# Kernel tuning notes

Measured on AMD Instinct MI355X. Metric: run time of the kernel, lower is better.

Reference implementation:

```python
import jax, jax.numpy as jnp
import numpy as np

R = 16            # grid resolution
WIN = 8           # window size (voxels per side)
NW3 = (R // WIN) ** 3   # number of windows = 8
WS = WIN ** 3           # tokens per window = 512
N = R ** 3              # active voxels = 4096
C = 512; H = 8; DH = C // H; L = 8; LAT = 8
NG = 4; VOX = 0.015625; OUTC = 14 * NG; MLP = 4 * C


def _radical_inverse(base, i):
    f = 1.0; r = 0.0
    while i > 0:
        f /= base; r += f * (i % base); i //= base
    return r


def _offset_perturbation():
    # hammersley_sequence(3, i, NG) = [i/NG, phi_2(i), phi_3(i)]
    p = np.array([[i / NG, _radical_inverse(2, i), _radical_inverse(3, i)] for i in range(NG)], np.float32)
    p = p * 2.0 - 1.0
    p = np.clip(p / VOX, -0.99, 0.99)
    return jnp.asarray(np.arctanh(p).astype(np.float32))  # [NG, 3]


def setup_inputs() -> dict:
    key = jax.random.key(0)
    ks = jax.random.split(key, 12)
    nw = R // WIN
    # window-major voxel ordering: dense 16^3 grid grouped into 8^3 windows
    win = np.stack(np.meshgrid(*[np.arange(nw)] * 3, indexing='ij'), -1).reshape(-1, 3)
    inner = np.stack(np.meshgrid(*[np.arange(WIN)] * 3, indexing='ij'), -1).reshape(-1, 3)
    xyz = (win[:, None, :] * WIN + inner[None, :, :]).reshape(-1, 3).astype(np.int32)
    coords = jnp.asarray(np.concatenate([np.zeros((N, 1), np.int32), xyz], axis=1))  # [N,4] (batch,x,y,z)
    s = 0.02
    return {
        'feats': jax.random.normal(ks[0], (N, LAT), jnp.float32),
        'coords': coords,
        'emb_x': jax.random.normal(ks[1], (1024, C // 3), jnp.float32) * s,
        'emb_y': jax.random.normal(ks[2], (1024, C // 3), jnp.float32) * s,
        'emb_z': jax.random.normal(ks[3], (1024, C - 2 * (C // 3)), jnp.float32) * s,
        'w_in': jax.random.normal(ks[4], (LAT, C), jnp.float32) * s,
        'b_in': jnp.zeros((C,), jnp.float32),
        'ln1_g': jnp.ones((L, C), jnp.float32), 'ln1_b': jnp.zeros((L, C), jnp.float32),
        'w_qkv': jax.random.normal(ks[5], (L, C, 3 * C), jnp.float32) * s,
        'b_qkv': jnp.zeros((L, 3 * C), jnp.float32),
        'w_o': jax.random.normal(ks[6], (L, C, C), jnp.float32) * s,
        'b_o': jnp.zeros((L, C), jnp.float32),
        'ln2_g': jnp.ones((L, C), jnp.float32), 'ln2_b': jnp.zeros((L, C), jnp.float32),
        'w_m1': jax.random.normal(ks[7], (L, C, MLP), jnp.float32) * s,
        'b_m1': jnp.zeros((L, MLP), jnp.float32),
        'w_m2': jax.random.normal(ks[8], (L, MLP, C), jnp.float32) * s,
        'b_m2': jnp.zeros((L, C), jnp.float32),
        'w_out': jax.random.normal(ks[9], (C, OUTC), jnp.float32) * s,
        'b_out': jnp.zeros((OUTC,), jnp.float32),
        'offset_perturb': _offset_perturbation(),
    }


def _ln(x, g, b, eps):
    m = jnp.mean(x, axis=-1, keepdims=True)
    v = jnp.var(x, axis=-1, keepdims=True)
    return (x - m) * jax.lax.rsqrt(v + eps) * g + b


def _forward(feats, coords, emb_x, emb_y, emb_z, w_in, b_in, ln1_g, ln1_b,
             w_qkv, b_qkv, w_o, b_o, ln2_g, ln2_b, w_m1, b_m1, w_m2, b_m2,
             w_out, b_out, offset_perturb):
    # input_layer + absolute position embedding (gather from 3 tables)
    h = feats @ w_in + b_in  # [N, C]
    pe = jnp.concatenate([emb_x[coords[:, 1]], emb_y[coords[:, 2]], emb_z[coords[:, 3]]], axis=-1)
    h = h + pe

    def block(h, p):
        l1g, l1b, wq, bq, wo, bo, l2g, l2b, w1, b1, w2, b2 = p
        a = _ln(h, l1g, l1b, 1e-6)
        qkv = (a @ wq + bq).reshape(NW3, WS, 3, H, DH)  # voxels are window-major
        q, k, v = qkv[:, :, 0], qkv[:, :, 1], qkv[:, :, 2]
        scores = jnp.einsum('wqhd,wkhd->whqk', q, k) / jnp.sqrt(jnp.float32(DH))
        attn = jax.nn.softmax(scores, axis=-1)
        o = jnp.einsum('whqk,wkhd->wqhd', attn, v).reshape(N, C)
        h = h + o @ wo + bo
        m = _ln(h, l2g, l2b, 1e-6)
        h = h + jax.nn.gelu(m @ w1 + b1) @ w2 + b2
        return h, None

    params = (ln1_g, ln1_b, w_qkv, b_qkv, w_o, b_o, ln2_g, ln2_b, w_m1, b_m1, w_m2, b_m2)
    h, _ = jax.lax.scan(block, h, params)

    # final non-affine layer_norm + out projection
    h = _ln(h, jnp.ones((C,), h.dtype), jnp.zeros((C,), h.dtype), 1e-5)
    out = h @ w_out + b_out  # [N, 56]

    # to_representation (single batch)
    xyz_base = (coords[:, 1:].astype(jnp.float32) + 0.5) / R  # [N, 3]
    off = out[:, 0:3 * NG].reshape(N, NG, 3) + offset_perturb
    off = jnp.tanh(off) / R * 0.5 * VOX
    _xyz = (xyz_base[:, None, :] + off).reshape(N * NG, 3)
    _fdc = out[:, 3 * NG:6 * NG].reshape(N * NG, 1, 3)
    _scal = out[:, 6 * NG:9 * NG].reshape(N * NG, 3)
    _rot = out[:, 9 * NG:13 * NG].reshape(N * NG, 4)
    _opa = out[:, 13 * NG:14 * NG].reshape(N * NG, 1)
    return _xyz, _fdc, _scal, _rot, _opa


def reference(feats, coords, emb_x, emb_y, emb_z, w_in, b_in, ln1_g, ln1_b,
              w_qkv, b_qkv, w_o, b_o, ln2_g, ln2_b, w_m1, b_m1, w_m2, b_m2,
              w_out, b_out, offset_perturb):
    return _forward(feats, coords, emb_x, emb_y, emb_z, w_in, b_in, ln1_g, ln1_b,
                    w_qkv, b_qkv, w_o, b_o, ln2_g, ln2_b, w_m1, b_m1, w_m2, b_m2,
                    w_out, b_out, offset_perturb)
```

## Files before the change

### kernel.cpp

```cpp
#include <hip/hip_runtime.h>
#include <stdint.h>

typedef unsigned short u16;
typedef short bf16x8 __attribute__((ext_vector_type(8)));
typedef float f32x4 __attribute__((ext_vector_type(4)));

#define NTOK 4096
#define CDIM 512
#define NHEAD 8
#define LAYERS 8
#define MLPD 2048
#define QKVD 1536

__device__ __forceinline__ u16 f2bf(float f){
  union { float f; unsigned u; } c; c.f = f;
  return (u16)((c.u + 0x7FFFu + ((c.u >> 16) & 1u)) >> 16);
}

__device__ __forceinline__ unsigned pack2(float a, float b){
  return (unsigned)f2bf(a) | ((unsigned)f2bf(b) << 16);
}

__device__ __forceinline__ void llds16(const void* g, void* l){
  __builtin_amdgcn_global_load_lds((const __attribute__((address_space(1))) void*)g,
                                   (__attribute__((address_space(3))) void*)l, 16, 0, 0);
}

__global__ void kt_transpose(const float* __restrict__ W, u16* __restrict__ Wt, int K, int N){
  __shared__ float tile[32][33];
  int l = blockIdx.z;
  W  += (size_t)l * K * N;
  Wt += (size_t)l * K * N;
  int k0 = blockIdx.y * 32, n0 = blockIdx.x * 32;
  int t = threadIdx.x;
  int r = t >> 3, c4 = (t & 7) << 2;
  float4 v = *(const float4*)&W[(size_t)(k0 + r) * N + n0 + c4];
  tile[r][c4 + 0] = v.x; tile[r][c4 + 1] = v.y; tile[r][c4 + 2] = v.z; tile[r][c4 + 3] = v.w;
  __syncthreads();
  ushort4 o;
  o.x = f2bf(tile[c4 + 0][r]);
  o.y = f2bf(tile[c4 + 1][r]);
  o.z = f2bf(tile[c4 + 2][r]);
  o.w = f2bf(tile[c4 + 3][r]);
  *(ushort4*)&Wt[(size_t)(n0 + r) * K + k0 + c4] = o;
}

__global__ void kt_embed(const float* __restrict__ feats, const int* __restrict__ coords,
                         const float* __restrict__ ex, const float* __restrict__ ey,
                         const float* __restrict__ ez, const float* __restrict__ w_in,
                         const float* __restrict__ b_in, float* __restrict__ h){
  __shared__ float fs[8];
  __shared__ int cc[3];
  int n = blockIdx.x, t = threadIdx.x;
  if (t < 8) fs[t] = feats[n * 8 + t];
  if (t == 8) { cc[0] = coords[n*4+1]; cc[1] = coords[n*4+2]; cc[2] = coords[n*4+3]; }
  __syncthreads();
  for (int c = t; c < CDIM; c += 256){
    float acc = b_in[c];
    #pragma unroll
    for (int i = 0; i < 8; i++) acc += fs[i] * w_in[i * CDIM + c];
    float pe;
    if (c < 170)      pe = ex[cc[0] * 170 + c];
    else if (c < 340) pe = ey[cc[1] * 170 + (c - 170)];
    else              pe = ez[cc[2] * 172 + (c - 340)];
    h[(size_t)n * CDIM + c] = acc + pe;
  }
}

__global__ void kt_ln(const float* __restrict__ h, const float* __restrict__ g,
                      const float* __restrict__ b, u16* __restrict__ out, float eps){
  int wave = threadIdx.x >> 6, lane = threadIdx.x & 63;
  int row = blockIdx.x * 4 + wave;
  const float* hr = h + (size_t)row * CDIM + lane * 8;
  float4 v0 = *(const float4*)hr, v1 = *(const float4*)(hr + 4);
  float x[8] = {v0.x, v0.y, v0.z, v0.w, v1.x, v1.y, v1.z, v1.w};
  float s = 0.f, q = 0.f;
  #pragma unroll
  for (int i = 0; i < 8; i++){ s += x[i]; q += x[i] * x[i]; }
  #pragma unroll
  for (int off = 32; off; off >>= 1){ s += __shfl_xor(s, off); q += __shfl_xor(q, off); }
  float mean = s * (1.0f / CDIM);
  float var  = q * (1.0f / CDIM) - mean * mean;
  float rr = rsqrtf(var + eps);
  int cb = lane * 8;
  u16 u[8];
  #pragma unroll
  for (int i = 0; i < 8; i++)
    u[i] = f2bf((x[i] - mean) * rr * g[cb + i] + b[cb + i]);
  uint4 pk;
  pk.x = (unsigned)u[0] | ((unsigned)u[1] << 16);
  pk.y = (unsigned)u[2] | ((unsigned)u[3] << 16);
  pk.z = (unsigned)u[4] | ((unsigned)u[5] << 16);
  pk.w = (unsigned)u[6] | ((unsigned)u[7] << 16);
  *(uint4*)&out[(size_t)row * CDIM + cb] = pk;
}

template<int BM, int BN, int MODE>
__global__ __launch_bounds__(256) void kt_gemm(
    const u16* __restrict__ A, const u16* __restrict__ Wt, const float* __restrict__ bias,
    u16* __restrict__ outb, float* __restrict__ hres, u16* __restrict__ vT, int N, int K)
{
  constexpr int MF = BM / 32;
  constexpr int NF = BN / 32;
  __shared__ __align__(16) u16 As[2][BM * 64];
  __shared__ __align__(16) u16 Bs[2][BN * 64];
  int tid = threadIdx.x, wave = tid >> 6, lane = tid & 63;
  int m0 = blockIdx.y * BM, n0 = blockIdx.x * BN;
  int wm = wave >> 1, wn = wave & 1;
  f32x4 acc[MF][NF];
  const f32x4 fzero = {0.f, 0.f, 0.f, 0.f};
  #pragma unroll
  for (int m = 0; m < MF; m++)
    #pragma unroll
    for (int n = 0; n < NF; n++) acc[m][n] = fzero;

  int srow = lane >> 3;
  int sblk = (lane & 7) ^ srow;
  const u16* gA = A  + (size_t)(m0 + wave * 8 + srow) * K + sblk * 8;
  const u16* gB = Wt + (size_t)(n0 + wave * 8 + srow) * K + sblk * 8;

  auto stage = [&](int buf, int kt){
    #pragma unroll
    for (int j = 0; j < BM / 32; j++)
      llds16(gA + (size_t)(j * 32) * K + kt, &As[buf][(j * 32 + wave * 8) * 64]);
    #pragma unroll
    for (int j = 0; j < BN / 32; j++)
      llds16(gB + (size_t)(j * 32) * K + kt, &Bs[buf][(j * 32 + wave * 8) * 64]);
  };

  int nk = K >> 6;
  stage(0, 0);
  __syncthreads();
  int rl = lane & 15, hg = lane >> 4;
  for (int t = 0; t < nk; ++t){
    int cur = t & 1;
    if (t + 1 < nk) stage(cur ^ 1, (t + 1) << 6);
    #pragma unroll
    for (int kk = 0; kk < 2; kk++){
      bf16x8 af[MF], bfr[NF];
      int bl = (kk << 2) + hg;
      #pragma unroll
      for (int m = 0; m < MF; m++){
        int row = wm * (BM / 2) + m * 16 + rl;
        af[m] = *(const bf16x8*)&As[cur][row * 64 + ((bl ^ (row & 7)) << 3)];
      }
      #pragma unroll
      for (int n = 0; n < NF; n++){
        int row = wn * (BN / 2) + n * 16 + rl;
        bfr[n] = *(const bf16x8*)&Bs[cur][row * 64 + ((bl ^ (row & 7)) << 3)];
      }
      #pragma unroll
      for (int m = 0; m < MF; m++)
        #pragma unroll
        for (int n = 0; n < NF; n++)
          acc[m][n] = __builtin_amdgcn_mfma_f32_16x16x32_bf16(af[m], bfr[n], acc[m][n], 0, 0, 0);
    }
    __syncthreads();
  }

  int cl = lane & 15, rg = lane >> 4;
  #pragma unroll
  for (int m = 0; m < MF; m++){
    int row0 = m0 + wm * (BM / 2) + m * 16 + rg * 4;
    #pragma unroll
    for (int n = 0; n < NF; n++){
      int col = n0 + wn * (BN / 2) + n * 16 + cl;
      float bb = bias[col];
      if (MODE == 1){
        #pragma unroll
        for (int r = 0; r < 4; r++){
          size_t idx = (size_t)(row0 + r) * N + col;
          hres[idx] += acc[m][n][r] + bb;
        }
      } else if (MODE == 2){
        #pragma unroll
        for (int r = 0; r < 4; r++){
          float x = acc[m][n][r] + bb;
          float t = 0.7978845608028654f * (x + 0.044715f * x * x * x);
          outb[(size_t)(row0 + r) * N + col] = f2bf(0.5f * x * (1.0f + tanhf(t)));
        }
      } else {
        if (col < 1024){
          #pragma unroll
          for (int r = 0; r < 4; r++)
            outb[(size_t)(row0 + r) * N + col] = f2bf(acc[m][n][r] + bb);
        } else {
          int dh = col - 1024;
          int win = row0 >> 9, tin = row0 & 511;
          ushort4 p;
          p.x = f2bf(acc[m][n][0] + bb);
          p.y = f2bf(acc[m][n][1] + bb);
          p.z = f2bf(acc[m][n][2] + bb);
          p.w = f2bf(acc[m][n][3] + bb);
          *(ushort4*)&vT[(size_t)(win * 512 + dh) * 512 + tin] = p;
        }
      }
    }
  }
}

__global__ __launch_bounds__(256) void kt_attn(const u16* __restrict__ qkv,
                                               const u16* __restrict__ vT,
                                               u16* __restrict__ o){
  int tid = threadIdx.x, wave = tid >> 6, lane = tid & 63;
  int task = blockIdx.x * 4 + wave;
  int qc = task & 31, head = (task >> 5) & 7, win = task >> 8;
  int rl = lane & 15, hg = lane >> 4;
  int qbase = win * 512 + qc * 16;
  const u16* qptr = qkv + (size_t)(qbase + rl) * QKVD + head * 64;
  const u16* kptr = qkv + (size_t)(win * 512) * QKVD + 512 + head * 64;
  const u16* vptr = vT + (size_t)(win * 512 + head * 64) * 512;

  bf16x8 qf0 = *(const bf16x8*)(qptr + hg * 8);
  bf16x8 qf1 = *(const bf16x8*)(qptr + 32 + hg * 8);

  const f32x4 fzero = {0.f, 0.f, 0.f, 0.f};
  f32x4 Oa[4] = {fzero, fzero, fzero, fzero};
  float mrun = -1e30f, lrun = 0.f;

  bf16x8 kA[2][2], vA[4], kB[2][2], vB[4];

  auto loadK = [&](int kt, bf16x8 kf[2][2]){
    #pragma unroll
    for (int c = 0; c < 2; c++)
      #pragma unroll
      for (int dk = 0; dk < 2; dk++)
        kf[c][dk] = *(const bf16x8*)(kptr + (size_t)(kt + c * 16 + rl) * QKVD + dk * 32 + hg * 8);
  };
  auto loadV = [&](int kt, bf16x8 vf[4]){
    #pragma unroll
    for (int d = 0; d < 4; d++)
      vf[d] = *(const bf16x8*)(vptr + (size_t)(d * 16 + rl) * 512 + kt + hg * 8);
  };

  auto process = [&](bf16x8 kf[2][2], bf16x8 vf[4]){
    f32x4 s0 = fzero, s1 = fzero;
    s0 = __builtin_amdgcn_mfma_f32_16x16x32_bf16(kf[0][0], qf0, s0, 0, 0, 0);
    s0 = __builtin_amdgcn_mfma_f32_16x16x32_bf16(kf[0][1], qf1, s0, 0, 0, 0);
    s1 = __builtin_amdgcn_mfma_f32_16x16x32_bf16(kf[1][0], qf0, s1, 0, 0, 0);
    s1 = __builtin_amdgcn_mfma_f32_16x16x32_bf16(kf[1][1], qf1, s1, 0, 0, 0);
    float v[8];
    #pragma unroll
    for (int r = 0; r < 4; r++){ v[r] = s0[r] * 0.125f; v[4 + r] = s1[r] * 0.125f; }
    float tmax = v[0];
    #pragma unroll
    for (int i = 1; i < 8; i++) tmax = fmaxf(tmax, v[i]);
    tmax = fmaxf(tmax, __shfl_xor(tmax, 16));
    tmax = fmaxf(tmax, __shfl_xor(tmax, 32));
    float mnew = fmaxf(mrun, tmax);
    float corr = __expf(mrun - mnew);
    mrun = mnew;
    float p[8], ps = 0.f;
    #pragma unroll
    for (int i = 0; i < 8; i++){ p[i] = __expf(v[i] - mnew); ps += p[i]; }
    ps += __shfl_xor(ps, 16);
    ps += __shfl_xor(ps, 32);
    lrun = lrun * corr + ps;
    float c0 = __shfl(corr, (hg << 2) + 0);
    float c1 = __shfl(corr, (hg << 2) + 1);
    float c2 = __shfl(corr, (hg << 2) + 2);
    float c3 = __shfl(corr, (hg << 2) + 3);
    #pragma unroll
    for (int d = 0; d < 4; d++){
      Oa[d][0] *= c0; Oa[d][1] *= c1; Oa[d][2] *= c2; Oa[d][3] *= c3;
    }
    unsigned pk00 = pack2(p[0], p[1]);
    unsigned pk01 = pack2(p[2], p[3]);
    unsigned pk10 = pack2(p[4], p[5]);
    unsigned pk11 = pack2(p[6], p[7]);
    int idx0 = rl | ((( hg << 1)      & 3) << 4);
    int idx1 = rl | ((((hg << 1) + 1) & 3) << 4);
    bool hiC = hg >= 2;
    unsigned W0a = __shfl(pk00, idx0), W0b = __shfl(pk10, idx0);
    unsigned W1a = __shfl(pk01, idx0), W1b = __shfl(pk11, idx0);
    unsigned W2a = __shfl(pk00, idx1), W2b = __shfl(pk10, idx1);
    unsigned W3a = __shfl(pk01, idx1), W3b = __shfl(pk11, idx1);
    uint4 W;
    W.x = hiC ? W0b : W0a;
    W.y = hiC ? W1b : W1a;
    W.z = hiC ? W2b : W2a;
    W.w = hiC ? W3b : W3a;
    bf16x8 pf;
    __builtin_memcpy(&pf, &W, 16);
    #pragma unroll
    for (int d = 0; d < 4; d++)
      Oa[d] = __builtin_amdgcn_mfma_f32_16x16x32_bf16(pf, vf[d], Oa[d], 0, 0, 0);
  };

  loadK(0, kA); loadV(0, vA);
  for (int kt = 0; kt < 512; kt += 64){
    loadK(kt + 32, kB); loadV(kt + 32, vB);
    process(kA, vA);
    if (kt + 64 < 512){ loadK(kt + 64, kA); loadV(kt + 64, vA); }
    process(kB, vB);
  }

  float l0 = __shfl(lrun, (hg << 2) + 0);
  float l1 = __shfl(lrun, (hg << 2) + 1);
  float l2 = __shfl(lrun, (hg << 2) + 2);
  float l3 = __shfl(lrun, (hg << 2) + 3);
  float li[4] = {1.f / l0, 1.f / l1, 1.f / l2, 1.f / l3};
  #pragma unroll
  for (int d = 0; d < 4; d++)
    #pragma unroll
    for (int r = 0; r < 4; r++){
      int row = qbase + (hg << 2) + r;
      o[(size_t)row * CDIM + head * 64 + d * 16 + rl] = f2bf(Oa[d][r] * li[r]);
    }
}

__global__ void kt_final(const float* __restrict__ h, const float* __restrict__ w_out,
                         const float* __restrict__ b_out, const int* __restrict__ coords,
                         const float* __restrict__ offp, float* __restrict__ out){
  __shared__ float lnv[CDIM];
  __shared__ float ov[56];
  int n = blockIdx.x, lane = threadIdx.x;
  const float* hr = h + (size_t)n * CDIM + lane * 8;
  float4 v0 = *(const float4*)hr, v1 = *(const float4*)(hr + 4);
  float x[8] = {v0.x, v0.y, v0.z, v0.w, v1.x, v1.y, v1.z, v1.w};
  float s = 0.f, q = 0.f;
  #pragma unroll
  for (int i = 0; i < 8; i++){ s += x[i]; q += x[i] * x[i]; }
  #pragma unroll
  for (int off = 32; off; off >>= 1){ s += __shfl_xor(s, off); q += __shfl_xor(q, off); }
  float mean = s * (1.0f / CDIM);
  float var  = q * (1.0f / CDIM) - mean * mean;
  float rr = rsqrtf(var + 1e-5f);
  #pragma unroll
  for (int i = 0; i < 8; i++) lnv[lane * 8 + i] = (x[i] - mean) * rr;
  __syncthreads();
  if (lane < 56){
    float a = b_out[lane];
    for (int k = 0; k < CDIM; k++) a += lnv[k] * w_out[k * 56 + lane];
    ov[lane] = a;
  }
  __syncthreads();
  if (lane < 12){
    int g = lane / 3, d = lane - g * 3;
    float base = ((float)coords[n * 4 + 1 + d] + 0.5f) * (1.0f / 16.0f);
    float t = tanhf(ov[lane] + offp[lane]);
    out[(size_t)n * 12 + lane] = base + t * 4.8828125e-4f;
    out[49152  + (size_t)n * 12 + lane] = ov[12 + lane];
    out[98304  + (size_t)n * 12 + lane] = ov[24 + lane];
  }
  if (lane < 16) out[147456 + (size_t)n * 16 + lane] = ov[36 + lane];
  if (lane < 4)  out[212992 + (size_t)n * 4  + lane] = ov[52 + lane];
}

extern "C" void kernel_launch(void* const* d_in, const int* in_sizes, int n_in,
                              void* d_out, int out_size, void* d_ws, size_t ws_size,
                              hipStream_t stream) {
  const float* feats = (const float*)d_in[0];
  const int*   coords = (const int*)d_in[1];
  const float* emb_x = (const float*)d_in[2];
  const float* emb_y = (const float*)d_in[3];
  const float* emb_z = (const float*)d_in[4];
  const float* w_in  = (const float*)d_in[5];
  const float* b_in  = (const float*)d_in[6];
  const float* ln1_g = (const float*)d_in[7];
  const float* ln1_b = (const float*)d_in[8];
  const float* w_qkv = (const float*)d_in[9];
  const float* b_qkv = (const float*)d_in[10];
  const float* w_o   = (const float*)d_in[11];
  const float* b_o   = (const float*)d_in[12];
  const float* ln2_g = (const float*)d_in[13];
  const float* ln2_b = (const float*)d_in[14];
  const float* w_m1  = (const float*)d_in[15];
  const float* b_m1  = (const float*)d_in[16];
  const float* w_m2  = (const float*)d_in[17];
  const float* b_m2  = (const float*)d_in[18];
  const float* w_out = (const float*)d_in[19];
  const float* b_out = (const float*)d_in[20];
  const float* offp  = (const float*)d_in[21];

  char* ws = (char*)d_ws;
  auto carve = [&](size_t bytes){ char* p = ws; ws += (bytes + 255) & ~(size_t)255; return p; };
  float* h   = (float*)carve((size_t)NTOK * CDIM * 4);
  u16* a     = (u16*)carve((size_t)NTOK * CDIM * 2);
  u16* qkvb  = (u16*)carve((size_t)NTOK * QKVD * 2);
  u16* vT    = (u16*)carve((size_t)NTOK * CDIM * 2);
  u16* ob    = (u16*)carve((size_t)NTOK * CDIM * 2);
  u16* ub    = (u16*)carve((size_t)NTOK * MLPD * 2);
  u16* wqkvT = (u16*)carve((size_t)LAYERS * QKVD * CDIM * 2);
  u16* woT   = (u16*)carve((size_t)LAYERS * CDIM * CDIM * 2);
  u16* wm1T  = (u16*)carve((size_t)LAYERS * MLPD * CDIM * 2);
  u16* wm2T  = (u16*)carve((size_t)LAYERS * CDIM * MLPD * 2);

  kt_transpose<<<dim3(QKVD/32, CDIM/32, LAYERS), 256, 0, stream>>>(w_qkv, wqkvT, CDIM, QKVD);
  kt_transpose<<<dim3(CDIM/32, CDIM/32, LAYERS), 256, 0, stream>>>(w_o,   woT,   CDIM, CDIM);
  kt_transpose<<<dim3(MLPD/32, CDIM/32, LAYERS), 256, 0, stream>>>(w_m1,  wm1T,  CDIM, MLPD);
  kt_transpose<<<dim3(CDIM/32, MLPD/32, LAYERS), 256, 0, stream>>>(w_m2,  wm2T,  MLPD, CDIM);
  kt_embed<<<NTOK, 256, 0, stream>>>(feats, coords, emb_x, emb_y, emb_z, w_in, b_in, h);

  for (int l = 0; l < LAYERS; ++l){
    kt_ln<<<NTOK/4, 256, 0, stream>>>(h, ln1_g + l*CDIM, ln1_b + l*CDIM, a, 1e-6f);
    kt_gemm<64,128,0><<<dim3(QKVD/128, NTOK/64), 256, 0, stream>>>(
        a, wqkvT + (size_t)l*QKVD*CDIM, b_qkv + l*QKVD, qkvb, nullptr, vT, QKVD, CDIM);
    kt_attn<<<512, 256, 0, stream>>>(qkvb, vT, ob);
    kt_gemm<64,64,1><<<dim3(CDIM/64, NTOK/64), 256, 0, stream>>>(
        ob, woT + (size_t)l*CDIM*CDIM, b_o + l*CDIM, nullptr, h, nullptr, CDIM, CDIM);
    kt_ln<<<NTOK/4, 256, 0, stream>>>(h, ln2_g + l*CDIM, ln2_b + l*CDIM, a, 1e-6f);
    kt_gemm<64,128,2><<<dim3(MLPD/128, NTOK/64), 256, 0, stream>>>(
        a, wm1T + (size_t)l*MLPD*CDIM, b_m1 + l*MLPD, ub, nullptr, nullptr, MLPD, CDIM);
    kt_gemm<64,64,1><<<dim3(CDIM/64, NTOK/64), 256, 0, stream>>>(
        ub, wm2T + (size_t)l*CDIM*MLPD, b_m2 + l*CDIM, nullptr, h, nullptr, CDIM, MLPD);
  }
  kt_final<<<NTOK, 64, 0, stream>>>(h, w_out, b_out, coords, offp, (float*)d_out);
}
```

Measured before the change: 978.3 us.

## Triple-buffer GEMM LDS pipeline and stage attention K/V through shared memory

The GEMM moves from double to triple buffering in LDS. It waits with explicit vmcnt counters and a single barrier per k-step instead of two __syncthreads. The attention kernel now groups four waves of one head and window per block. Those waves share K/V tiles loaded into swizzled LDS through a triple-buffered async global_load_lds pipeline, replacing per-wave redundant global register loads. This is meant to cut redundant global traffic and barrier stalls, at the cost of more LDS use and reliance on hand-tuned vmcnt correctness.

```diff
diff --git a/kernel.cpp b/kernel.cpp
--- a/kernel.cpp
+++ b/kernel.cpp
@@ -24,6 +24,14 @@
 __device__ __forceinline__ void llds16(const void* g, void* l){
   __builtin_amdgcn_global_load_lds((const __attribute__((address_space(1))) void*)g,
                                    (__attribute__((address_space(3))) void*)l, 16, 0, 0);
+}
+
+template<int N> __device__ __forceinline__ void wait_vmcnt(){
+  if constexpr (N == 0) asm volatile("s_waitcnt vmcnt(0)" ::: "memory");
+  else if constexpr (N == 2) asm volatile("s_waitcnt vmcnt(2)" ::: "memory");
+  else if constexpr (N == 4) asm volatile("s_waitcnt vmcnt(4)" ::: "memory");
+  else if constexpr (N == 6) asm volatile("s_waitcnt vmcnt(6)" ::: "memory");
+  else static_assert(N == 0 || N == 2 || N == 4 || N == 6, "unsupported vmcnt");
 }
 
 __global__ void kt_transpose(const float* __restrict__ W, u16* __restrict__ Wt, int K, int N){
@@ -102,8 +110,9 @@
 {
   constexpr int MF = BM / 32;
   constexpr int NF = BN / 32;
-  __shared__ __align__(16) u16 As[2][BM * 64];
-  __shared__ __align__(16) u16 Bs[2][BN * 64];
+  constexpr int S = MF + NF;
+  __shared__ __align__(16) u16 As[3][BM * 64];
+  __shared__ __align__(16) u16 Bs[3][BN * 64];
   int tid = threadIdx.x, wave = tid >> 6, lane = tid & 63;
   int m0 = blockIdx.y * BM, n0 = blockIdx.x * BN;
   int wm = wave >> 1, wn = wave & 1;
@@ -121,20 +130,23 @@
 
   auto stage = [&](int buf, int kt){
     #pragma unroll
-    for (int j = 0; j < BM / 32; j++)
+    for (int j = 0; j < MF; j++)
       llds16(gA + (size_t)(j * 32) * K + kt, &As[buf][(j * 32 + wave * 8) * 64]);
     #pragma unroll
-    for (int j = 0; j < BN / 32; j++)
+    for (int j = 0; j < NF; j++)
       llds16(gB + (size_t)(j * 32) * K + kt, &Bs[buf][(j * 32 + wave * 8) * 64]);
   };
 
   int nk = K >> 6;
   stage(0, 0);
-  __syncthreads();
+  stage(1, 64);
   int rl = lane & 15, hg = lane >> 4;
   for (int t = 0; t < nk; ++t){
-    int cur = t & 1;
-    if (t + 1 < nk) stage(cur ^ 1, (t + 1) << 6);
+    int cur = t % 3;
+    if (t + 1 < nk) wait_vmcnt<S>(); else wait_vmcnt<0>();
+    __builtin_amdgcn_s_barrier();
+    asm volatile("" ::: "memory");
+    if (t + 2 < nk) stage((t + 2) % 3, (t + 2) << 6);
     #pragma unroll
     for (int kk = 0; kk < 2; kk++){
       bf16x8 af[MF], bfr[NF];
@@ -155,7 +167,6 @@
         for (int n = 0; n < NF; n++)
           acc[m][n] = __builtin_amdgcn_mfma_f32_16x16x32_bf16(af[m], bfr[n], acc[m][n], 0, 0, 0);
     }
-    __syncthreads();
   }
 
   int cl = lane & 15, rg = lane >> 4;
@@ -202,14 +213,26 @@
 __global__ __launch_bounds__(256) void kt_attn(const u16* __restrict__ qkv,
                                                const u16* __restrict__ vT,
                                                u16* __restrict__ o){
+  __shared__ __align__(16) u16 Ks[3][32 * 64];
+  __shared__ __align__(16) u16 Vs[3][64 * 32];
   int tid = threadIdx.x, wave = tid >> 6, lane = tid & 63;
-  int task = blockIdx.x * 4 + wave;
-  int qc = task & 31, head = (task >> 5) & 7, win = task >> 8;
+  int bx = blockIdx.x;
+  int win = bx >> 6, head = (bx >> 3) & 7, q8 = bx & 7;
   int rl = lane & 15, hg = lane >> 4;
-  int qbase = win * 512 + qc * 16;
-  const u16* qptr = qkv + (size_t)(qbase + rl) * QKVD + head * 64;
-  const u16* kptr = qkv + (size_t)(win * 512) * QKVD + 512 + head * 64;
-  const u16* vptr = vT + (size_t)(win * 512 + head * 64) * 512;
+  int qbase = win * 512 + q8 * 64 + wave * 16;
+  const u16* qptr  = qkv + (size_t)(qbase + rl) * QKVD + head * 64;
+  const u16* kbase = qkv + (size_t)(win * 512) * QKVD + 512 + head * 64;
+  const u16* vbase = vT + (size_t)(win * 512 + head * 64) * 512;
+
+  int krow = tid >> 3;
+  const u16* gK = kbase + (size_t)krow * QKVD + (((tid & 7) ^ (krow & 7)) << 3);
+  int vrow = tid >> 2;
+  const u16* gV = vbase + (size_t)vrow * 512 + (((tid & 3) ^ (vrow & 3)) << 3);
+
+  auto stage = [&](int buf, int kt){
+    llds16(gK + (size_t)kt * QKVD, &Ks[buf][tid * 8]);
+    llds16(gV + kt, &Vs[buf][tid * 8]);
+  };
 
   bf16x8 qf0 = *(const bf16x8*)(qptr + hg * 8);
   bf16x8 qf1 = *(const bf16x8*)(qptr + 32 + hg * 8);
@@ -218,22 +241,30 @@
   f32x4 Oa[4] = {fzero, fzero, fzero, fzero};
   float mrun = -1e30f, lrun = 0.f;
 
-  bf16x8 kA[2][2], vA[4], kB[2][2], vB[4];
-
-  auto loadK = [&](int kt, bf16x8 kf[2][2]){
+  stage(0, 0);
+  stage(1, 32);
+  for (int t = 0; t < 16; ++t){
+    int cur = t % 3;
+    if (t + 1 < 16) wait_vmcnt<2>(); else wait_vmcnt<0>();
+    __builtin_amdgcn_s_barrier();
+    asm volatile("" ::: "memory");
+    if (t + 2 < 16) stage((t + 2) % 3, (t + 2) * 32);
+
+    bf16x8 kf[2][2];
     #pragma unroll
     for (int c = 0; c < 2; c++)
       #pragma unroll
-      for (int dk = 0; dk < 2; dk++)
-        kf[c][dk] = *(const bf16x8*)(kptr + (size_t)(kt + c * 16 + rl) * QKVD + dk * 32 + hg * 8);
-  };
-  auto loadV = [&](int kt, bf16x8 vf[4]){
-    #pragma unroll
-    for (int d = 0; d < 4; d++)
-      vf[d] = *(const bf16x8*)(vptr + (size_t)(d * 16 + rl) * 512 + kt + hg * 8);
-  };
-
-  auto process = [&](bf16x8 kf[2][2], bf16x8 vf[4]){
+      for (int dk = 0; dk < 2; dk++){
+        int row = c * 16 + rl;
+        kf[c][dk] = *(const bf16x8*)&Ks[cur][row * 64 + ((((dk << 2) + hg) ^ (rl & 7)) << 3)];
+      }
+    bf16x8 vf[4];
+    #pragma unroll
+    for (int d = 0; d < 4; d++){
+      int row = d * 16 + rl;
+      vf[d] = *(const bf16x8*)&Vs[cur][row * 32 + ((hg ^ (rl & 3)) << 3)];
+    }
+
     f32x4 s0 = fzero, s1 = fzero;
     s0 = __builtin_amdgcn_mfma_f32_16x16x32_bf16(kf[0][0], qf0, s0, 0, 0, 0);
     s0 = __builtin_amdgcn_mfma_f32_16x16x32_bf16(kf[0][1], qf1, s0, 0, 0, 0);
@@ -285,14 +316,6 @@
     #pragma unroll
     for (int d = 0; d < 4; d++)
       Oa[d] = __builtin_amdgcn_mfma_f32_16x16x32_bf16(pf, vf[d], Oa[d], 0, 0, 0);
-  };
-
-  loadK(0, kA); loadV(0, vA);
-  for (int kt = 0; kt < 512; kt += 64){
-    loadK(kt + 32, kB); loadV(kt + 32, vB);
-    process(kA, vA);
-    if (kt + 64 < 512){ loadK(kt + 64, kA); loadV(kt + 64, vA); }
-    process(kB, vB);
   }
 
   float l0 = __shfl(lrun, (hg << 2) + 0);
```

After: 959.1 us. 2.0% less time.
